# Performance work log

Hardware: AMD Instinct MI355X
Metric: run time of the kernel (lower is better)

Reference implementation:

```python
import jax, jax.numpy as jnp
import numpy as np

B, N_PER, N_TOOL, D, T = 64, 4096, 1000, 128, 50
SCALE = 50.0  # self.scale_pcl_val


def setup_inputs() -> dict:
    key = jax.random.key(0)
    ks = jax.random.split(key, 9)
    return {
        "x_feat": jax.random.normal(ks[0], (B * N_PER, D), jnp.float32),
        "pos": jax.random.normal(ks[1], (B * N_PER, 3), jnp.float32),
        "tool_idx": jax.random.randint(ks[2], (B, N_TOOL), 0, N_PER, jnp.int32),
        "W1": jax.random.normal(ks[3], (D, D), jnp.float32) * 0.05,
        "b1": jnp.zeros((D,), jnp.float32),
        "W2": jax.random.normal(ks[4], (D, D), jnp.float32) * 0.05,
        "b2": jnp.zeros((D,), jnp.float32),
        "W3": jax.random.normal(ks[5], (D, 3 * T), jnp.float32) * 0.05,
        "b3": jnp.zeros((3 * T,), jnp.float32),
    }


def _kabsch(xyz, flow):
    # xyz, flow: [B, N, 3]; fit rigid transform mapping xyz -> xyz + flow (Kabsch/SVD)
    y = xyz + flow
    mu_x = xyz.mean(axis=1, keepdims=True)
    mu_y = y.mean(axis=1, keepdims=True)
    xc = xyz - mu_x
    yc = y - mu_y
    H = jnp.einsum('bni,bnj->bij', xc, yc)  # [B,3,3] covariance
    U, S, Vt = jnp.linalg.svd(H)
    d = jnp.sign(jnp.linalg.det(U @ Vt))  # reflection fix, [B]
    Dm = jnp.stack([jnp.ones_like(d), jnp.ones_like(d), d], axis=-1)  # [B,3]
    R = (U * Dm[:, None, :]) @ Vt  # [B,3,3]
    return jnp.einsum('bni,bij->bnj', xc, R) + mu_y  # transformed points


def reference(x_feat, pos, tool_idx, W1, b1, W2, b2, W3, b3):
    # MLP([128,128,128,flow_dim]) head (eval mode: dropout off)
    h = jax.nn.relu(x_feat @ W1 + b1)
    h = jax.nn.relu(h @ W2 + b2)
    flow_per_pt = (h @ W3 + b3).reshape(B, N_PER, T, 3)

    pos_s = (pos * SCALE).reshape(B, N_PER, 3)  # data['pos'] * scale_pcl_val
    idx3 = tool_idx[:, :, None]
    xyz0 = jnp.take_along_axis(pos_s, idx3, axis=1)  # [B, N_TOOL, 3]
    flows = jnp.take_along_axis(flow_per_pt, tool_idx[:, :, None, None], axis=1)  # [B, N_TOOL, T, 3]
    flows_t = jnp.moveaxis(flows, 2, 0)  # [T, B, N_TOOL, 3]

    def step(xyz, flow):
        new_xyz = _kabsch(xyz, flow)
        return new_xyz, (new_xyz - xyz, flow)

    _, (flow_traj, before_svd) = jax.lax.scan(step, xyz0, flows_t)
    flow_traj = jnp.moveaxis(flow_traj, 0, 1)      # [B, T, N_TOOL, 3]
    before_svd = jnp.moveaxis(before_svd, 0, 1)    # [B, T, N_TOOL, 3]
    return flow_traj, before_svd
```

## Files before the change

### kernel.cpp

```cpp
#include <hip/hip_runtime.h>
#include <cstddef>

#define HB 64
#define HN_PER 4096
#define HN_TOOL 1000
#define HD 128
#define HT 50
#define HSCALE 50.0f

typedef _Float16 f16x8 __attribute__((ext_vector_type(8)));
typedef float f32x4 __attribute__((ext_vector_type(4)));

constexpr int TILE_M = 64;
constexpr int APITCH = 136;
constexpr int SPITCH = 204;

constexpr int W1_BASE = 0;
constexpr int W2_BASE = 16384;
constexpr int W3_BASE = 32768;

constexpr int XC0_F = 26624;
constexpr int C0_F  = XC0_F + HB * HN_TOOL * 3;
constexpr int BT_F  = C0_F + HB * 9;
constexpr int MT_F  = BT_F + HB * HT * 12;

__device__ __forceinline__ float wave_red_sum(float v)
{
#define DPP_ADD(ctrl)                                                          \
    v += __builtin_bit_cast(float, __builtin_amdgcn_update_dpp(                \
             0, __builtin_bit_cast(int, v), (ctrl), 0xF, 0xF, true));
    DPP_ADD(0x128)
    DPP_ADD(0x124)
    DPP_ADD(0x122)
    DPP_ADD(0x121)
#undef DPP_ADD
    v += __shfl_xor(v, 16, 64);
    v += __shfl_xor(v, 32, 64);
    return v;
}

__global__ __launch_bounds__(256) void prep_kernel(
    const float* __restrict__ pos,
    const int* __restrict__ tool_idx,
    const float* __restrict__ W1, const float* __restrict__ W2,
    const float* __restrict__ W3,
    _Float16* __restrict__ wsh, float* __restrict__ wsf)
{
    __shared__ float red[4][6];
    const int blk = blockIdx.x;
    const int tid = threadIdx.x;

    if (blk < 64) {
        const int b = blk;
        const int lane = tid & 63, wv = tid >> 6;
        const int nb = tid * 4;
        const bool act = nb < HN_TOOL;

        float xv[4], yv[4], zv[4];
        if (act) {
            const int4 i4 = *(const int4*)(tool_idx + b * HN_TOOL + nb);
            const int pi[4] = {i4.x, i4.y, i4.z, i4.w};
#pragma unroll
            for (int s = 0; s < 4; ++s) {
                const float* pp = pos + (size_t)(b * HN_PER + pi[s]) * 3;
                xv[s] = pp[0] * HSCALE;
                yv[s] = pp[1] * HSCALE;
                zv[s] = pp[2] * HSCALE;
            }
        }
        float s0 = 0.f, s1 = 0.f, s2 = 0.f;
        if (act) {
#pragma unroll
            for (int s = 0; s < 4; ++s) { s0 += xv[s]; s1 += yv[s]; s2 += zv[s]; }
        }
        s0 = wave_red_sum(s0); s1 = wave_red_sum(s1); s2 = wave_red_sum(s2);
        if (lane == 0) { red[wv][0] = s0; red[wv][1] = s1; red[wv][2] = s2; }
        __syncthreads();
        const float invN = 1.0f / HN_TOOL;
        const float mux = (red[0][0] + red[1][0] + red[2][0] + red[3][0]) * invN;
        const float muy = (red[0][1] + red[1][1] + red[2][1] + red[3][1]) * invN;
        const float muz = (red[0][2] + red[1][2] + red[2][2] + red[3][2]) * invN;
        __syncthreads();

        float xx = 0.f, xy = 0.f, xz = 0.f, yy = 0.f, yz = 0.f, zz = 0.f;
        if (act) {
            float o[12];
#pragma unroll
            for (int s = 0; s < 4; ++s) {
                const float x = xv[s] - mux, y = yv[s] - muy, z = zv[s] - muz;
                o[3 * s + 0] = x; o[3 * s + 1] = y; o[3 * s + 2] = z;
                xx += x * x; xy += x * y; xz += x * z;
                yy += y * y; yz += y * z; zz += z * z;
            }
            float4* dst = (float4*)(wsf + XC0_F + (size_t)b * (HN_TOOL * 3) + nb * 3);
            dst[0] = *(float4*)&o[0];
            dst[1] = *(float4*)&o[4];
            dst[2] = *(float4*)&o[8];
        }
        float c6[6] = {xx, xy, xz, yy, yz, zz};
#pragma unroll
        for (int v = 0; v < 6; ++v) c6[v] = wave_red_sum(c6[v]);
        if (lane == 0) {
#pragma unroll
            for (int v = 0; v < 6; ++v) red[wv][v] = c6[v];
        }
        __syncthreads();
        if (tid == 0) {
            float g[6];
#pragma unroll
            for (int v = 0; v < 6; ++v)
                g[v] = red[0][v] + red[1][v] + red[2][v] + red[3][v];
            float* c0 = wsf + C0_F + b * 9;
            c0[0] = g[0]; c0[1] = g[1]; c0[2] = g[2];
            c0[3] = g[1]; c0[4] = g[3]; c0[5] = g[4];
            c0[6] = g[2]; c0[7] = g[4]; c0[8] = g[5];
        }
    } else if (blk < 90) {
        const int lane = tid & 63;
        const int f = (blk - 64) * 4 + (tid >> 6);
        const float* W; int ncols, base, fi;
        if (f < 32)       { W = W1; ncols = 128; base = W1_BASE; fi = f; }
        else if (f < 64)  { W = W2; ncols = 128; base = W2_BASE; fi = f - 32; }
        else              { W = W3; ncols = 150; base = W3_BASE; fi = f - 64; }
        const int nt = fi >> 2, kc = fi & 3;
        const int col = nt * 16 + (lane & 15);
        const int k0 = kc * 32 + (lane >> 4) * 8;
        f16x8 v;
#pragma unroll
        for (int j = 0; j < 8; ++j)
            v[j] = (col < ncols) ? (_Float16)W[(size_t)(k0 + j) * ncols + col]
                                 : (_Float16)0.f;
        *(f16x8*)(wsh + ((size_t)(base + (fi * 64 + lane) * 8))) = v;
    } else {
        const float4 z4 = {0.f, 0.f, 0.f, 0.f};
        float4* bt4 = (float4*)(wsf + BT_F);
        for (int i = tid; i < (HB * HT * 12) / 4; i += 256) bt4[i] = z4;
    }
}

__global__ __launch_bounds__(256) void mlp_mfma_kernel(
    const float* __restrict__ x_feat,
    const int* __restrict__ tool_idx,
    const _Float16* __restrict__ Wsw,
    const float* __restrict__ b1, const float* __restrict__ b2,
    const float* __restrict__ b3,
    float* __restrict__ out2, float* __restrict__ wsf)
{
    __shared__ __align__(16) char smem[HT * SPITCH * 4];
    _Float16 (*hA)[APITCH] = (_Float16 (*)[APITCH])smem;
    float* stage = (float*)smem;

    const int tid = threadIdx.x;
    const int lane = tid & 63, w = tid >> 6;
    const int lm = lane & 15, quad = lane >> 4;
    const int m0 = w * 16;
    const int bx = blockIdx.x;
    const int b  = blockIdx.y;
    const int n0 = bx * TILE_M;

    {
        const int i = tid >> 2;
        const int c0 = (tid & 3) * 32;
        const int n = n0 + i;
        const int nc = (n < HN_TOOL) ? n : (HN_TOOL - 1);
        const int p = tool_idx[b * HN_TOOL + nc];
        const float4* src =
            (const float4*)(x_feat + (size_t)(b * HN_PER + p) * HD + c0);
#pragma unroll
        for (int fq = 0; fq < 4; ++fq) {
            const float4 u = src[2 * fq], v = src[2 * fq + 1];
            f16x8 h = {(_Float16)u.x, (_Float16)u.y, (_Float16)u.z, (_Float16)u.w,
                       (_Float16)v.x, (_Float16)v.y, (_Float16)v.z, (_Float16)v.w};
            *(f16x8*)&hA[i][c0 + fq * 8] = h;
        }
    }
    __syncthreads();

#pragma unroll
    for (int layer = 0; layer < 2; ++layer) {
        const _Float16* wb = Wsw + (layer ? W2_BASE : W1_BASE);
        const float* bias = layer ? b2 : b1;
        f16x8 afr[4];
#pragma unroll
        for (int kc = 0; kc < 4; ++kc)
            afr[kc] = *(const f16x8*)&hA[m0 + lm][kc * 32 + quad * 8];
        f32x4 acc[8];
#pragma unroll
        for (int nt = 0; nt < 8; ++nt) acc[nt] = (f32x4){0.f, 0.f, 0.f, 0.f};
#pragma unroll
        for (int kc = 0; kc < 4; ++kc)
#pragma unroll
            for (int nt = 0; nt < 8; ++nt) {
                const f16x8 bf = *(const f16x8*)(wb + (size_t)((nt * 4 + kc) * 64 + lane) * 8);
                acc[nt] = __builtin_amdgcn_mfma_f32_16x16x32_f16(afr[kc], bf, acc[nt], 0, 0, 0);
            }
#pragma unroll
        for (int nt = 0; nt < 8; ++nt) {
            const float bb = bias[nt * 16 + lm];
#pragma unroll
            for (int r = 0; r < 4; ++r)
                hA[m0 + quad * 4 + r][nt * 16 + lm] =
                    (_Float16)fmaxf(acc[nt][r] + bb, 0.f);
        }
    }

    {
        f16x8 afr[4];
#pragma unroll
        for (int kc = 0; kc < 4; ++kc)
            afr[kc] = *(const f16x8*)&hA[m0 + lm][kc * 32 + quad * 8];
        __syncthreads();
        f32x4 acc[10];
#pragma unroll
        for (int nt = 0; nt < 10; ++nt) acc[nt] = (f32x4){0.f, 0.f, 0.f, 0.f};
#pragma unroll
        for (int kc = 0; kc < 4; ++kc)
#pragma unroll
            for (int nt = 0; nt < 10; ++nt) {
                const f16x8 bf = *(const f16x8*)(Wsw + W3_BASE + (size_t)((nt * 4 + kc) * 64 + lane) * 8);
                acc[nt] = __builtin_amdgcn_mfma_f32_16x16x32_f16(afr[kc], bf, acc[nt], 0, 0, 0);
            }
#pragma unroll
        for (int nt = 0; nt < 10; ++nt) {
            const int j = nt * 16 + lm;
            if (j < 150) {
                const float bb = b3[j];
                const int t = j / 3, c = j - 3 * t;
#pragma unroll
                for (int r = 0; r < 4; ++r)
                    stage[t * SPITCH + (m0 + quad * 4 + r) * 3 + c] = acc[nt][r] + bb;
            }
        }
    }
    __syncthreads();

    const int V = (bx == 15) ? (HN_TOOL - 15 * TILE_M) : TILE_M;
    const int nf4 = (V * 3) >> 2;
    {
        float* ob = out2 + (size_t)b * HT * (HN_TOOL * 3) + (size_t)n0 * 3;
        for (int t = w; t < HT; t += 4) {
            if (lane < nf4) {
                const f32x4 v = *(const f32x4*)&stage[t * SPITCH + lane * 4];
                __builtin_nontemporal_store(
                    v, (f32x4*)(ob + (size_t)t * (HN_TOOL * 3)) + lane);
            }
        }
    }

    if (tid < 4 * HT) {
        const int t = tid >> 2, part = tid & 3;
        const float* xc = wsf + XC0_F + (size_t)b * (HN_TOOL * 3) + (size_t)n0 * 3;
        float S[12];
#pragma unroll
        for (int v = 0; v < 12; ++v) S[v] = 0.f;
#pragma unroll
        for (int rr = 0; rr < 16; ++rr) {
            const int nl = part * 16 + rr;
            if (n0 + nl < HN_TOOL) {
                const float x = xc[3 * nl + 0], y = xc[3 * nl + 1], z = xc[3 * nl + 2];
                const float fx = stage[t * SPITCH + 3 * nl + 0];
                const float fy = stage[t * SPITCH + 3 * nl + 1];
                const float fz = stage[t * SPITCH + 3 * nl + 2];
                S[0] += x * fx; S[1] += x * fy; S[2] += x * fz;
                S[3] += y * fx; S[4] += y * fy; S[5] += y * fz;
                S[6] += z * fx; S[7] += z * fy; S[8] += z * fz;
                S[9] += fx; S[10] += fy; S[11] += fz;
            }
        }
#pragma unroll
        for (int v = 0; v < 12; ++v) {
            S[v] += __shfl_xor(S[v], 1, 64);
            S[v] += __shfl_xor(S[v], 2, 64);
        }
        if (part == 0) {
            float* btp = wsf + BT_F + ((size_t)b * HT + t) * 12;
#pragma unroll
            for (int v = 0; v < 12; ++v) atomicAdd(btp + v, S[v]);
        }
    }
}

__global__ __launch_bounds__(64) void compose_kernel(float* __restrict__ ws)
{
    const int b = threadIdx.x;
    float C0[9], P[9];
#pragma unroll
    for (int v = 0; v < 9; ++v) C0[v] = ws[C0_F + b * 9 + v];
    P[0] = 1.f; P[1] = 0.f; P[2] = 0.f;
    P[3] = 0.f; P[4] = 1.f; P[5] = 0.f;
    P[6] = 0.f; P[7] = 0.f; P[8] = 1.f;

    const float invN = 1.0f / HN_TOOL;
    const float* bt = ws + BT_F + (size_t)b * HT * 12;
    float* mt = ws + MT_F + (size_t)b * HT * 12;

    float4 n0 = *(const float4*)(bt);
    float4 n1 = *(const float4*)(bt + 4);
    float4 n2 = *(const float4*)(bt + 8);

    for (int t = 0; t < HT; ++t) {
        const float Bv[12] = {n0.x, n0.y, n0.z, n0.w, n1.x, n1.y, n1.z, n1.w,
                              n2.x, n2.y, n2.z, n2.w};
        if (t + 1 < HT) {
            const float* nb = bt + (t + 1) * 12;
            n0 = *(const float4*)(nb);
            n1 = *(const float4*)(nb + 4);
            n2 = *(const float4*)(nb + 8);
        }
        float G[9];
#pragma unroll
        for (int i = 0; i < 3; ++i)
#pragma unroll
            for (int j = 0; j < 3; ++j)
                G[i * 3 + j] = C0[i * 3 + 0] * P[0 * 3 + j] +
                               C0[i * 3 + 1] * P[1 * 3 + j] +
                               C0[i * 3 + 2] * P[2 * 3 + j] + Bv[i * 3 + j];
        float X[9];
#pragma unroll
        for (int i = 0; i < 3; ++i)
#pragma unroll
            for (int j = 0; j < 3; ++j)
                X[i * 3 + j] = P[0 * 3 + i] * G[0 * 3 + j] +
                               P[1 * 3 + i] * G[1 * 3 + j] +
                               P[2 * 3 + i] * G[2 * 3 + j];
        const float scl = 3.0f * __builtin_amdgcn_rcpf(X[0] + X[4] + X[8]);
#pragma unroll
        for (int v = 0; v < 9; ++v) X[v] *= scl;
#pragma unroll
        for (int it = 0; it < 2; ++it) {
            float C[9];
            C[0] =  (X[4] * X[8] - X[5] * X[7]);
            C[1] = -(X[3] * X[8] - X[5] * X[6]);
            C[2] =  (X[3] * X[7] - X[4] * X[6]);
            C[3] = -(X[1] * X[8] - X[2] * X[7]);
            C[4] =  (X[0] * X[8] - X[2] * X[6]);
            C[5] = -(X[0] * X[7] - X[1] * X[6]);
            C[6] =  (X[1] * X[5] - X[2] * X[4]);
            C[7] = -(X[0] * X[5] - X[2] * X[3]);
            C[8] =  (X[0] * X[4] - X[1] * X[3]);
            const float det = X[0] * C[0] + X[1] * C[1] + X[2] * C[2];
            const float rdet = 0.5f * __builtin_amdgcn_rcpf(det);
#pragma unroll
            for (int v = 0; v < 9; ++v) X[v] = 0.5f * X[v] + C[v] * rdet;
        }
        float Pn[9];
#pragma unroll
        for (int i = 0; i < 3; ++i)
#pragma unroll
            for (int j = 0; j < 3; ++j)
                Pn[i * 3 + j] = P[i * 3 + 0] * X[0 * 3 + j] +
                                P[i * 3 + 1] * X[1 * 3 + j] +
                                P[i * 3 + 2] * X[2 * 3 + j];
        float4 m0, m1, m2;
        m0.x = Pn[0] - P[0]; m0.y = Pn[1] - P[1]; m0.z = Pn[2] - P[2];
        m0.w = Pn[3] - P[3]; m1.x = Pn[4] - P[4]; m1.y = Pn[5] - P[5];
        m1.z = Pn[6] - P[6]; m1.w = Pn[7] - P[7]; m2.x = Pn[8] - P[8];
        m2.y = Bv[9] * invN; m2.z = Bv[10] * invN; m2.w = Bv[11] * invN;
        float* mo = mt + t * 12;
        *(float4*)(mo) = m0;
        *(float4*)(mo + 4) = m1;
        *(float4*)(mo + 8) = m2;
#pragma unroll
        for (int v = 0; v < 9; ++v) P[v] = Pn[v];
    }
}

__global__ __launch_bounds__(256) void apply_kernel(
    const float* __restrict__ ws, float* __restrict__ out1)
{
    __shared__ float M[12];
    const int t = blockIdx.x, b = blockIdx.y;
    const int tid = threadIdx.x;
    if (tid < 12) M[tid] = ws[MT_F + (size_t)(b * HT + t) * 12 + tid];
    __syncthreads();

    const int nb = tid * 4;
    if (nb < HN_TOOL) {
        const float4* xc4 =
            (const float4*)(ws + XC0_F + (size_t)b * (HN_TOOL * 3) + nb * 3);
        float in12[12], o12[12];
        *(float4*)&in12[0] = xc4[0];
        *(float4*)&in12[4] = xc4[1];
        *(float4*)&in12[8] = xc4[2];
#pragma unroll
        for (int k = 0; k < 4; ++k) {
            const float x = in12[3 * k], y = in12[3 * k + 1], z = in12[3 * k + 2];
            o12[3 * k + 0] = x * M[0] + y * M[3] + z * M[6] + M[9];
            o12[3 * k + 1] = x * M[1] + y * M[4] + z * M[7] + M[10];
            o12[3 * k + 2] = x * M[2] + y * M[5] + z * M[8] + M[11];
        }
        f32x4* ot = (f32x4*)(out1 + ((size_t)(b * HT + t) * HN_TOOL) * 3 + nb * 3);
        __builtin_nontemporal_store(*(f32x4*)&o12[0], ot + 0);
        __builtin_nontemporal_store(*(f32x4*)&o12[4], ot + 1);
        __builtin_nontemporal_store(*(f32x4*)&o12[8], ot + 2);
    }
}

extern "C" void kernel_launch(void* const* d_in, const int* in_sizes, int n_in,
                              void* d_out, int out_size, void* d_ws, size_t ws_size,
                              hipStream_t stream)
{
    const float* x_feat   = (const float*)d_in[0];
    const float* pos      = (const float*)d_in[1];
    const int*   tool_idx = (const int*)d_in[2];
    const float* W1 = (const float*)d_in[3];
    const float* b1 = (const float*)d_in[4];
    const float* W2 = (const float*)d_in[5];
    const float* b2 = (const float*)d_in[6];
    const float* W3 = (const float*)d_in[7];
    const float* b3 = (const float*)d_in[8];

    float* out1 = (float*)d_out;
    float* out2 = out1 + (size_t)HB * HT * HN_TOOL * 3;
    _Float16* wsw = (_Float16*)d_ws;
    float* wsf = (float*)d_ws;

    prep_kernel<<<91, 256, 0, stream>>>(pos, tool_idx, W1, W2, W3, wsw, wsf);
    mlp_mfma_kernel<<<dim3(16, HB), 256, 0, stream>>>(
        x_feat, tool_idx, wsw, b1, b2, b3, out2, wsf);
    compose_kernel<<<1, 64, 0, stream>>>(wsf);
    apply_kernel<<<dim3(HT, HB), 256, 0, stream>>>(wsf, out1);
}
```

Measured before the change: 330.7 us.

## Halve MLP tile size and replace atomics with per-tile partials reduced in compose

The MLP kernel now uses 32-row tiles with 128 threads, doubling the grid to 32x64 blocks for better occupancy. Per-(b,t) statistics are written as per-tile partial sums instead of global atomicAdd, which also removes the zeroing block in prep. The compose kernel becomes one block per batch that first reduces the partials in parallel into shared memory and then runs the serial recurrence on one thread. It trades atomic contention and a single-block compose for more workspace traffic and more, smaller blocks.

Measured after the change: 335.5 us. Within noise of the previous version (+1.4%).

```diff
diff --git a/kernel.cpp b/kernel.cpp
--- a/kernel.cpp
+++ b/kernel.cpp
@@ -11,9 +11,10 @@
 typedef _Float16 f16x8 __attribute__((ext_vector_type(8)));
 typedef float f32x4 __attribute__((ext_vector_type(4)));
 
-constexpr int TILE_M = 64;
+constexpr int TILE_M = 32;
+constexpr int NBX   = 32;
 constexpr int APITCH = 136;
-constexpr int SPITCH = 204;
+constexpr int SPITCH = 100;
 
 constexpr int W1_BASE = 0;
 constexpr int W2_BASE = 16384;
@@ -23,6 +24,7 @@
 constexpr int C0_F  = XC0_F + HB * HN_TOOL * 3;
 constexpr int BT_F  = C0_F + HB * 9;
 constexpr int MT_F  = BT_F + HB * HT * 12;
+constexpr int PART_F = MT_F + HB * HT * 12;
 
 __device__ __forceinline__ float wave_red_sum(float v)
 {
@@ -115,7 +117,7 @@
             c0[3] = g[1]; c0[4] = g[3]; c0[5] = g[4];
             c0[6] = g[2]; c0[7] = g[4]; c0[8] = g[5];
         }
-    } else if (blk < 90) {
+    } else {
         const int lane = tid & 63;
         const int f = (blk - 64) * 4 + (tid >> 6);
         const float* W; int ncols, base, fi;
@@ -131,14 +133,10 @@
             v[j] = (col < ncols) ? (_Float16)W[(size_t)(k0 + j) * ncols + col]
                                  : (_Float16)0.f;
         *(f16x8*)(wsh + ((size_t)(base + (fi * 64 + lane) * 8))) = v;
-    } else {
-        const float4 z4 = {0.f, 0.f, 0.f, 0.f};
-        float4* bt4 = (float4*)(wsf + BT_F);
-        for (int i = tid; i < (HB * HT * 12) / 4; i += 256) bt4[i] = z4;
-    }
-}
-
-__global__ __launch_bounds__(256) void mlp_mfma_kernel(
+    }
+}
+
+__global__ __launch_bounds__(128) void mlp_mfma_kernel(
     const float* __restrict__ x_feat,
     const int* __restrict__ tool_idx,
     const _Float16* __restrict__ Wsw,
@@ -204,13 +202,13 @@
         }
     }
 
+    f32x4 acc[10];
     {
         f16x8 afr[4];
 #pragma unroll
         for (int kc = 0; kc < 4; ++kc)
             afr[kc] = *(const f16x8*)&hA[m0 + lm][kc * 32 + quad * 8];
         __syncthreads();
-        f32x4 acc[10];
 #pragma unroll
         for (int nt = 0; nt < 10; ++nt) acc[nt] = (f32x4){0.f, 0.f, 0.f, 0.f};
 #pragma unroll
@@ -220,25 +218,27 @@
                 const f16x8 bf = *(const f16x8*)(Wsw + W3_BASE + (size_t)((nt * 4 + kc) * 64 + lane) * 8);
                 acc[nt] = __builtin_amdgcn_mfma_f32_16x16x32_f16(afr[kc], bf, acc[nt], 0, 0, 0);
             }
-#pragma unroll
-        for (int nt = 0; nt < 10; ++nt) {
-            const int j = nt * 16 + lm;
-            if (j < 150) {
-                const float bb = b3[j];
-                const int t = j / 3, c = j - 3 * t;
-#pragma unroll
-                for (int r = 0; r < 4; ++r)
-                    stage[t * SPITCH + (m0 + quad * 4 + r) * 3 + c] = acc[nt][r] + bb;
-            }
+    }
+
+#pragma unroll
+    for (int nt = 0; nt < 10; ++nt) {
+        const int j = nt * 16 + lm;
+        if (j < 150) {
+            const float bb = b3[j];
+            const int t = j / 3, c = j - 3 * t;
+#pragma unroll
+            for (int r = 0; r < 4; ++r)
+                stage[t * SPITCH + (m0 + quad * 4 + r) * 3 + c] =
+                    acc[nt][r] + bb;
         }
     }
     __syncthreads();
 
-    const int V = (bx == 15) ? (HN_TOOL - 15 * TILE_M) : TILE_M;
+    const int V = (bx == NBX - 1) ? (HN_TOOL - (NBX - 1) * TILE_M) : TILE_M;
     const int nf4 = (V * 3) >> 2;
     {
         float* ob = out2 + (size_t)b * HT * (HN_TOOL * 3) + (size_t)n0 * 3;
-        for (int t = w; t < HT; t += 4) {
+        for (int t = w; t < HT; t += 2) {
             if (lane < nf4) {
                 const f32x4 v = *(const f32x4*)&stage[t * SPITCH + lane * 4];
                 __builtin_nontemporal_store(
@@ -247,8 +247,8 @@
         }
     }
 
-    if (tid < 4 * HT) {
-        const int t = tid >> 2, part = tid & 3;
+    if (tid < 2 * HT) {
+        const int t = tid >> 1, part = tid & 1;
         const float* xc = wsf + XC0_F + (size_t)b * (HN_TOOL * 3) + (size_t)n0 * 3;
         float S[12];
 #pragma unroll
@@ -257,7 +257,8 @@
         for (int rr = 0; rr < 16; ++rr) {
             const int nl = part * 16 + rr;
             if (n0 + nl < HN_TOOL) {
-                const float x = xc[3 * nl + 0], y = xc[3 * nl + 1], z = xc[3 * nl + 2];
+                const float x = xc[3 * nl + 0], y = xc[3 * nl + 1],
+                            z = xc[3 * nl + 2];
                 const float fx = stage[t * SPITCH + 3 * nl + 0];
                 const float fy = stage[t * SPITCH + 3 * nl + 1];
                 const float fz = stage[t * SPITCH + 3 * nl + 2];
@@ -268,21 +269,36 @@
             }
         }
 #pragma unroll
-        for (int v = 0; v < 12; ++v) {
-            S[v] += __shfl_xor(S[v], 1, 64);
-            S[v] += __shfl_xor(S[v], 2, 64);
-        }
+        for (int v = 0; v < 12; ++v) S[v] += __shfl_xor(S[v], 1, 64);
         if (part == 0) {
-            float* btp = wsf + BT_F + ((size_t)b * HT + t) * 12;
-#pragma unroll
-            for (int v = 0; v < 12; ++v) atomicAdd(btp + v, S[v]);
-        }
-    }
-}
-
-__global__ __launch_bounds__(64) void compose_kernel(float* __restrict__ ws)
-{
-    const int b = threadIdx.x;
+            float* pp = wsf + PART_F + (((size_t)b * HT + t) * 12) * NBX + bx;
+#pragma unroll
+            for (int v = 0; v < 12; ++v) pp[v * NBX] = S[v];
+        }
+    }
+}
+
+__global__ __launch_bounds__(256) void composeR_kernel(float* __restrict__ ws)
+{
+    __shared__ float btl[HT * 12];
+    const int b = blockIdx.x;
+    const int tid = threadIdx.x;
+
+    for (int o = tid; o < HT * 12; o += 256) {
+        const float4* p =
+            (const float4*)(ws + PART_F + ((size_t)b * HT * 12 + o) * NBX);
+        float s = 0.f;
+#pragma unroll
+        for (int q = 0; q < NBX / 4; ++q) {
+            const float4 a = p[q];
+            s += (a.x + a.y) + (a.z + a.w);
+        }
+        btl[o] = s;
+    }
+    __syncthreads();
+
+    if (tid != 0) return;
+
     float C0[9], P[9];
 #pragma unroll
     for (int v = 0; v < 9; ++v) C0[v] = ws[C0_F + b * 9 + v];
@@ -291,22 +307,10 @@
     P[6] = 0.f; P[7] = 0.f; P[8] = 1.f;
 
     const float invN = 1.0f / HN_TOOL;
-    const float* bt = ws + BT_F + (size_t)b * HT * 12;
     float* mt = ws + MT_F + (size_t)b * HT * 12;
 
-    float4 n0 = *(const float4*)(bt);
-    float4 n1 = *(const float4*)(bt + 4);
-    float4 n2 = *(const float4*)(bt + 8);
-
     for (int t = 0; t < HT; ++t) {
-        const float Bv[12] = {n0.x, n0.y, n0.z, n0.w, n1.x, n1.y, n1.z, n1.w,
-                              n2.x, n2.y, n2.z, n2.w};
-        if (t + 1 < HT) {
-            const float* nb = bt + (t + 1) * 12;
-            n0 = *(const float4*)(nb);
-            n1 = *(const float4*)(nb + 4);
-            n2 = *(const float4*)(nb + 8);
-        }
+        const float* Bv = &btl[t * 12];
         float G[9];
 #pragma unroll
         for (int i = 0; i < 3; ++i)
@@ -415,9 +419,9 @@
     _Float16* wsw = (_Float16*)d_ws;
     float* wsf = (float*)d_ws;
 
-    prep_kernel<<<91, 256, 0, stream>>>(pos, tool_idx, W1, W2, W3, wsw, wsf);
-    mlp_mfma_kernel<<<dim3(16, HB), 256, 0, stream>>>(
+    prep_kernel<<<90, 256, 0, stream>>>(pos, tool_idx, W1, W2, W3, wsw, wsf);
+    mlp_mfma_kernel<<<dim3(NBX, HB), 128, 0, stream>>>(
         x_feat, tool_idx, wsw, b1, b2, b3, out2, wsf);
-    compose_kernel<<<1, 64, 0, stream>>>(wsf);
+    composeR_kernel<<<HB, 256, 0, stream>>>(wsf);
     apply_kernel<<<dim3(HT, HB), 256, 0, stream>>>(wsf, out1);
 }
```
